# Kernel tuning notes

Measured on AMD Instinct MI355X. Metric: run time of the kernel, lower is better.

## Reference

```python
import jax, jax.numpy as jnp
import numpy as np

B, T, D = 4, 2048, 768
H = 12
DH = D // H
DFF = 3072
EPS = 1e-5


def _layernorm(x, g, b):
    mu = jnp.mean(x, axis=-1, keepdims=True)
    var = jnp.var(x, axis=-1, keepdims=True)
    return (x - mu) * jax.lax.rsqrt(var + EPS) * g + b


def setup_inputs() -> dict:
    key = jax.random.key(0)
    ks = jax.random.split(key, 12)
    s = lambda fan_in: 1.0 / np.sqrt(fan_in)
    return {
        "x": jax.random.normal(ks[0], (B, T, D), dtype=jnp.float32),
        "ln1_g": jnp.ones((D,), jnp.float32),
        "ln1_b": jnp.zeros((D,), jnp.float32),
        "w_qkv": jax.random.uniform(ks[1], (D, 3 * D), jnp.float32, -s(D), s(D)),
        "b_qkv": jax.random.uniform(ks[2], (3 * D,), jnp.float32, -s(D), s(D)),
        "w_proj": jax.random.uniform(ks[3], (D, D), jnp.float32, -s(D), s(D)),
        "b_proj": jax.random.uniform(ks[4], (D,), jnp.float32, -s(D), s(D)),
        "ln2_g": jnp.ones((D,), jnp.float32),
        "ln2_b": jnp.zeros((D,), jnp.float32),
        "w_ff1": jax.random.uniform(ks[5], (D, DFF), jnp.float32, -s(D), s(D)),
        "b_ff1": jax.random.uniform(ks[6], (DFF,), jnp.float32, -s(D), s(D)),
        "w_ff2": jax.random.uniform(ks[7], (DFF, D), jnp.float32, -s(DFF), s(DFF)),
        "b_ff2": jax.random.uniform(ks[8], (D,), jnp.float32, -s(DFF), s(DFF)),
    }


def reference(x, ln1_g, ln1_b, w_qkv, b_qkv, w_proj, b_proj,
              ln2_g, ln2_b, w_ff1, b_ff1, w_ff2, b_ff2):
    # --- attention sublayer ---
    h = _layernorm(x, ln1_g, ln1_b)
    qkv = h @ w_qkv + b_qkv                       # [B,T,3D]
    q, k, v = jnp.split(qkv, 3, axis=-1)
    q = q.reshape(B, T, H, DH).transpose(0, 2, 1, 3)  # [B,H,T,DH]
    k = k.reshape(B, T, H, DH).transpose(0, 2, 1, 3)
    v = v.reshape(B, T, H, DH).transpose(0, 2, 1, 3)
    att = jnp.einsum('bhqd,bhkd->bhqk', q, k) / jnp.sqrt(jnp.float32(DH))
    causal = jnp.tril(jnp.ones((T, T), dtype=bool))
    att = jnp.where(causal, att, -jnp.inf)
    att = jax.nn.softmax(att, axis=-1)
    out = jnp.einsum('bhqk,bhkd->bhqd', att, v)    # [B,H,T,DH]
    out = out.transpose(0, 2, 1, 3).reshape(B, T, D)
    x = x + out @ w_proj + b_proj
    # --- MLP sublayer ---
    h2 = _layernorm(x, ln2_g, ln2_b)
    h2 = jax.nn.gelu(h2 @ w_ff1 + b_ff1, approximate=False)
    x = x + h2 @ w_ff2 + b_ff2
    return x
```

## Files before the change

### kernel.cpp

```cpp
#include <hip/hip_runtime.h>
#include <cstdint>
#include <cstddef>

typedef unsigned short u16;
typedef unsigned int u32;
typedef __attribute__((ext_vector_type(8))) short s16x8;
typedef __attribute__((ext_vector_type(4))) float f32x4;

#define NB 4
#define NT 2048
#define ND 768
#define NH 12
#define NDH 64
#define NFF 3072
#define NM (NB*NT)

__device__ __forceinline__ u16 f2b(float f){
  union { float f; unsigned u; } c; c.f = f;
  unsigned r = c.u + 0x7fffu + ((c.u >> 16) & 1u);
  return (u16)(r >> 16);
}

__device__ __forceinline__ f32x4 mfma16(s16x8 a, s16x8 b, f32x4 c){
  return __builtin_amdgcn_mfma_f32_16x16x32_bf16(a, b, c, 0, 0, 0);
}

__device__ __forceinline__ void stage16(u16* lds, const u16* g){
  __builtin_amdgcn_global_load_lds(
      (const __attribute__((address_space(1))) unsigned int*)g,
      (__attribute__((address_space(3))) unsigned int*)lds,
      16, 0, 0);
}

__device__ __forceinline__ float gelu_f(float v){
  const float x = v * 0.70710678118654752f;
  const float ax = fabsf(x);
  const float t = 1.f / (1.f + 0.3275911f * ax);
  const float y = t * (0.254829592f + t * (-0.284496736f + t * (1.421413741f
                + t * (-1.453152027f + t * 1.061405429f))));
  float er = 1.f - y * __expf(-ax * ax);
  er = copysignf(er, x);
  return 0.5f * v * (1.f + er);
}

__global__ __launch_bounds__(256) void transpose_bf16(
    const float* __restrict__ in, u16* __restrict__ out, int K, int N)
{
  __shared__ float tile[32][33];
  const int n0 = blockIdx.x * 32, k0 = blockIdx.y * 32;
  const int tx = threadIdx.x, ty = threadIdx.y;
  #pragma unroll
  for (int i = 0; i < 32; i += 8)
    tile[ty + i][tx] = in[(size_t)(k0 + ty + i) * N + n0 + tx];
  __syncthreads();
  #pragma unroll
  for (int i = 0; i < 32; i += 8)
    out[(size_t)(n0 + ty + i) * K + k0 + tx] = f2b(tile[tx][ty + i]);
}

__global__ __launch_bounds__(256) void ln_kernel(
    const float* __restrict__ x, const float* __restrict__ g,
    const float* __restrict__ b, u16* __restrict__ out)
{
  const int row = blockIdx.x;
  const int t = threadIdx.x;
  const float* xr = x + (size_t)row * ND;
  float v0 = xr[t], v1 = xr[t + 256], v2 = xr[t + 512];
  float s = v0 + v1 + v2;
  float ss = v0*v0 + v1*v1 + v2*v2;
  #pragma unroll
  for (int o = 32; o; o >>= 1) { s += __shfl_xor(s, o, 64); ss += __shfl_xor(ss, o, 64); }
  __shared__ float red[8];
  const int w = t >> 6;
  if ((t & 63) == 0) { red[w] = s; red[4 + w] = ss; }
  __syncthreads();
  s  = red[0] + red[1] + red[2] + red[3];
  ss = red[4] + red[5] + red[6] + red[7];
  const float mu = s * (1.f / ND);
  const float var = ss * (1.f / ND) - mu * mu;
  const float rinv = rsqrtf(var + 1e-5f);
  u16* orow = out + (size_t)row * ND;
  orow[t]       = f2b((v0 - mu) * rinv * g[t]       + b[t]);
  orow[t + 256] = f2b((v1 - mu) * rinv * g[t + 256] + b[t + 256]);
  orow[t + 512] = f2b((v2 - mu) * rinv * g[t + 512] + b[t + 512]);
}

template<int EPI, int BM>
__global__ __launch_bounds__(256, (BM == 128) ? 3 : 4) void gemm_bt(
    const u16* __restrict__ A, const u16* __restrict__ Bt,
    const float* __restrict__ bias, const float* __restrict__ res,
    void* __restrict__ o0, void* __restrict__ o1, void* __restrict__ o2,
    const int M, const int N, const int K)
{
  constexpr int MI = BM / 64;
  __shared__ u16 As[3][BM * 32];
  __shared__ u16 Bs[3][128 * 32];
  const int tid = threadIdx.x;
  const int lane = tid & 63, wid = tid >> 6;
  const int wr = wid >> 1, wc = wid & 1;
  const int lg = lane >> 4, lm = lane & 15;
  const int bm = blockIdx.x * BM, bn = blockIdx.y * 128;

  f32x4 acc[2 * MI][4] = {};

  const int srow = tid >> 2;
  const int schunk = (tid & 3) ^ ((tid >> 3) & 3);
  const u16* ApT = A  + (size_t)(bm + srow) * K + schunk * 8;
  const u16* BpT = Bt + (size_t)(bn + srow) * K + schunk * 8;
  const size_t rs64 = (size_t)64 * K;
  const int woff = wid * 512;
  const int fswz = (lm >> 1) & 3;

  const int nt = K >> 5;

  #pragma unroll
  for (int p = 0; p < 2; ++p) {
    const int k0 = p << 5;
    stage16(&As[p][woff], ApT + k0);
    if (BM == 128) stage16(&As[p][woff + 2048], ApT + rs64 + k0);
    stage16(&Bs[p][woff],        BpT + k0);
    stage16(&Bs[p][woff + 2048], BpT + rs64 + k0);
  }

  for (int t = 0; t < nt; ++t) {
    if (t < nt - 1) {
      if (BM == 128) asm volatile("s_waitcnt vmcnt(4)" ::: "memory");
      else           asm volatile("s_waitcnt vmcnt(3)" ::: "memory");
    } else {
      asm volatile("s_waitcnt vmcnt(0)" ::: "memory");
    }
    __builtin_amdgcn_s_barrier();
    __builtin_amdgcn_sched_barrier(0);
    if (t + 2 < nt) {
      const int k0 = (t + 2) << 5;
      const int wb = (t + 2) % 3;
      stage16(&As[wb][woff], ApT + k0);
      if (BM == 128) stage16(&As[wb][woff + 2048], ApT + rs64 + k0);
      stage16(&Bs[wb][woff],        BpT + k0);
      stage16(&Bs[wb][woff + 2048], BpT + rs64 + k0);
    }
    __builtin_amdgcn_sched_barrier(0);
    const int rb = t % 3;
    s16x8 af[2 * MI], bf[4];
    #pragma unroll
    for (int i = 0; i < 2 * MI; i++)
      af[i] = *(const s16x8*)&As[rb][(wr * (BM / 2) + i * 16 + lm) * 32 + ((lg ^ fswz) * 8)];
    #pragma unroll
    for (int j = 0; j < 4; j++)
      bf[j] = *(const s16x8*)&Bs[rb][(wc * 64 + j * 16 + lm) * 32 + ((lg ^ fswz) * 8)];
    #pragma unroll
    for (int i = 0; i < 2 * MI; i++)
      #pragma unroll
      for (int j = 0; j < 4; j++)
        acc[i][j] = mfma16(af[i], bf[j], acc[i][j]);
  }

  #pragma unroll
  for (int i = 0; i < 2 * MI; i++)
    #pragma unroll
    for (int j = 0; j < 4; j++) {
      const int col = bn + wc * 64 + j * 16 + lm;
      const float bb = bias[col];
      #pragma unroll
      for (int r = 0; r < 4; r++) {
        const int row = bm + wr * (BM / 2) + i * 16 + lg * 4 + r;
        float v = acc[i][j][r] + bb;
        if (EPI == 0) {
          u16* dst; int rem;
          if (col < ND)            { dst = (u16*)o0; rem = col; v *= 0.125f; }
          else if (col < 2 * ND)   { dst = (u16*)o1; rem = col - ND; }
          else                     { dst = (u16*)o2; rem = col - 2 * ND; }
          const int hh = rem >> 6, dh = rem & 63;
          const int bb2 = row >> 11, tt = row & 2047;
          dst[(((size_t)bb2 * NH + hh) * NT + tt) * NDH + dh] = f2b(v);
        } else if (EPI == 1) {
          ((float*)o0)[(size_t)row * ND + col] = v + res[(size_t)row * ND + col];
        } else if (EPI == 2) {
          ((u16*)o0)[(size_t)row * NFF + col] = f2b(gelu_f(v));
        } else {
          ((float*)o0)[(size_t)row * ND + col] = v + res[(size_t)row * ND + col];
        }
      }
    }
}

__global__ __launch_bounds__(256,2) void attn_kernel(
    const u16* __restrict__ Q, const u16* __restrict__ Kg,
    const u16* __restrict__ V, u16* __restrict__ O)
{
  const int pairIdx = blockIdx.y;
  const int bh = blockIdx.x;
  const int b = bh / NH, h = bh % NH;
  const int tid = threadIdx.x;
  const int lane = tid & 63, w = tid >> 6;
  const int lg = lane >> 4, lm = lane & 15;
  const int sr = tid >> 3;
  const int sc = (tid & 7) * 8;

  __shared__ u16 Ks[64 * 64];
  __shared__ u16 Vt[64 * 64];
  __shared__ u16 Ps[4][16 * 64];

  const u16* Qb = Q  + (size_t)bh * NT * NDH;
  const u16* Kb = Kg + (size_t)bh * NT * NDH;
  const u16* Vb = V  + (size_t)bh * NT * NDH;

  for (int half = 0; half < 2; ++half) {
    const int si = half ? (31 - pairIdx) : pairIdx;
    const int q0 = si * 64;
    const int ktmax = si;

    const s16x8 qf0 = *(const s16x8*)&Qb[(size_t)(q0 + w * 16 + lm) * NDH + lg * 8];
    const s16x8 qf1 = *(const s16x8*)&Qb[(size_t)(q0 + w * 16 + lm) * NDH + 32 + lg * 8];

    f32x4 oacc[4] = {};
    float m = -INFINITY, l = 0.f;

    s16x8 kva = *(const s16x8*)&Kb[(size_t)sr * NDH + sc];
    s16x8 kvb = *(const s16x8*)&Kb[(size_t)(sr + 32) * NDH + sc];
    s16x8 vva = *(const s16x8*)&Vb[(size_t)sr * NDH + sc];
    s16x8 vvb = *(const s16x8*)&Vb[(size_t)(sr + 32) * NDH + sc];

    for (int kt = 0; kt <= ktmax; ++kt) {
      __syncthreads();
      *(s16x8*)&Ks[sr * 64 + (sc ^ ((sr & 7) << 3))] = kva;
      *(s16x8*)&Ks[(sr + 32) * 64 + (sc ^ ((sr & 7) << 3))] = kvb;
      #pragma unroll
      for (int e = 0; e < 8; ++e)
        Vt[(sc + e) * 64 + (sr ^ ((tid & 7) << 3))] = (u16)vva[e];
      #pragma unroll
      for (int e = 0; e < 8; ++e)
        Vt[(sc + e) * 64 + ((sr + 32) ^ ((tid & 7) << 3))] = (u16)vvb[e];
      __syncthreads();

      if (kt < ktmax) {
        const u16* Kn = Kb + (size_t)(kt + 1) * 64 * NDH;
        const u16* Vn = Vb + (size_t)(kt + 1) * 64 * NDH;
        kva = *(const s16x8*)&Kn[(size_t)sr * NDH + sc];
        kvb = *(const s16x8*)&Kn[(size_t)(sr + 32) * NDH + sc];
        vva = *(const s16x8*)&Vn[(size_t)sr * NDH + sc];
        vvb = *(const s16x8*)&Vn[(size_t)(sr + 32) * NDH + sc];
      }

      f32x4 sv[4];
      #pragma unroll
      for (int n = 0; n < 4; ++n) {
        const int krow = (n * 16 + lm) * 64;
        const int swz = (lm & 7) << 3;
        s16x8 kf0 = *(const s16x8*)&Ks[krow + ((lg * 8) ^ swz)];
        s16x8 kf1 = *(const s16x8*)&Ks[krow + ((32 + lg * 8) ^ swz)];
        f32x4 s4 = {};
        s4 = mfma16(kf0, qf0, s4);
        s4 = mfma16(kf1, qf1, s4);
        sv[n] = s4;
      }

      if (kt == ktmax) {
        #pragma unroll
        for (int n = 0; n < 4; ++n)
          #pragma unroll
          for (int r = 0; r < 4; ++r)
            if (n * 16 + lg * 4 + r > w * 16 + lm) sv[n][r] = -INFINITY;
      }

      float mx = -INFINITY;
      #pragma unroll
      for (int n = 0; n < 4; ++n)
        #pragma unroll
        for (int r = 0; r < 4; ++r) mx = fmaxf(mx, sv[n][r]);
      mx = fmaxf(mx, __shfl_xor(mx, 16));
      mx = fmaxf(mx, __shfl_xor(mx, 32));
      const float mnew = fmaxf(m, mx);
      const float alpha = __expf(m - mnew);
      m = mnew;

      float rs = 0.f;
      u32 pk[4][2];
      #pragma unroll
      for (int n = 0; n < 4; ++n) {
        const float p0 = __expf(sv[n][0] - mnew);
        const float p1 = __expf(sv[n][1] - mnew);
        const float p2 = __expf(sv[n][2] - mnew);
        const float p3 = __expf(sv[n][3] - mnew);
        rs += (p0 + p1) + (p2 + p3);
        pk[n][0] = (u32)f2b(p0) | ((u32)f2b(p1) << 16);
        pk[n][1] = (u32)f2b(p2) | ((u32)f2b(p3) << 16);
      }
      rs += __shfl_xor(rs, 16);
      rs += __shfl_xor(rs, 32);
      l = l * alpha + rs;

      #pragma unroll
      for (int n = 0; n < 4; ++n) {
        const int idx0 = lm * 64 + ((n * 16 + lg * 4) ^ ((lm & 7) << 3));
        *(u32*)&Ps[w][idx0] = pk[n][0];
        *(u32*)&Ps[w][idx0 + 2] = pk[n][1];
      }

      float av[4];
      #pragma unroll
      for (int r = 0; r < 4; ++r) av[r] = __shfl(alpha, lg * 4 + r);
      #pragma unroll
      for (int d = 0; d < 4; ++d)
        #pragma unroll
        for (int r = 0; r < 4; ++r) oacc[d][r] *= av[r];

      #pragma unroll
      for (int kh = 0; kh < 2; ++kh) {
        const s16x8 pf = *(const s16x8*)&Ps[w][lm * 64 + ((kh * 32 + lg * 8) ^ ((lm & 7) << 3))];
        #pragma unroll
        for (int dt = 0; dt < 4; ++dt) {
          const int g = (2 * dt + (lm >> 3)) & 7;
          const s16x8 vf = *(const s16x8*)&Vt[(dt * 16 + lm) * 64 + (((kh * 4 + lg) ^ g) << 3)];
          oacc[dt] = mfma16(pf, vf, oacc[dt]);
        }
      }
    }

    float lv[4];
    #pragma unroll
    for (int r = 0; r < 4; ++r) lv[r] = 1.f / __shfl(l, lg * 4 + r);
    #pragma unroll
    for (int dt = 0; dt < 4; ++dt)
      #pragma unroll
      for (int r = 0; r < 4; ++r) {
        const int qg = q0 + w * 16 + lg * 4 + r;
        O[((size_t)b * NT + qg) * ND + h * NDH + dt * 16 + lm] = f2b(oacc[dt][r] * lv[r]);
      }
  }
}

extern "C" void kernel_launch(void* const* d_in, const int* in_sizes, int n_in,
                              void* d_out, int out_size, void* d_ws, size_t ws_size,
                              hipStream_t stream)
{
  const float* x      = (const float*)d_in[0];
  const float* ln1_g  = (const float*)d_in[1];
  const float* ln1_b  = (const float*)d_in[2];
  const float* w_qkv  = (const float*)d_in[3];
  const float* b_qkv  = (const float*)d_in[4];
  const float* w_proj = (const float*)d_in[5];
  const float* b_proj = (const float*)d_in[6];
  const float* ln2_g  = (const float*)d_in[7];
  const float* ln2_b  = (const float*)d_in[8];
  const float* w_ff1  = (const float*)d_in[9];
  const float* b_ff1  = (const float*)d_in[10];
  const float* w_ff2  = (const float*)d_in[11];
  const float* b_ff2  = (const float*)d_in[12];

  char* ws = (char*)d_ws;
  u16*   wt_qkv = (u16*)(ws + 0);
  u16*   wt_proj= (u16*)(ws + 3538944);
  u16*   wt_ff1 = (u16*)(ws + 4718592);
  u16*   wt_ff2 = (u16*)(ws + 9437184);
  u16*   hbuf   = (u16*)(ws + 14155776);
  u16*   qbuf   = (u16*)(ws + 26738688);
  u16*   kbuf   = (u16*)(ws + 39321600);
  u16*   vbuf   = (u16*)(ws + 51904512);
  u16*   aobuf  = (u16*)(ws + 64487424);
  float* x1     = (float*)(ws + 77070336);
  u16*   h2buf  = (u16*)(ws + 102236160);
  u16*   ff1buf = hbuf;

  transpose_bf16<<<dim3(2304/32,  768/32), dim3(32,8), 0, stream>>>(w_qkv,  wt_qkv,  768, 2304);
  transpose_bf16<<<dim3( 768/32,  768/32), dim3(32,8), 0, stream>>>(w_proj, wt_proj, 768,  768);
  transpose_bf16<<<dim3(3072/32,  768/32), dim3(32,8), 0, stream>>>(w_ff1,  wt_ff1,  768, 3072);
  transpose_bf16<<<dim3( 768/32, 3072/32), dim3(32,8), 0, stream>>>(w_ff2,  wt_ff2, 3072,  768);

  ln_kernel<<<NM, 256, 0, stream>>>(x, ln1_g, ln1_b, hbuf);
  gemm_bt<0,128><<<dim3(NM/128, 2304/128), 256, 0, stream>>>(hbuf, wt_qkv, b_qkv, nullptr,
                                                             qbuf, kbuf, vbuf, NM, 2304, ND);
  attn_kernel<<<dim3(NB*NH, 16), 256, 0, stream>>>(qbuf, kbuf, vbuf, aobuf);
  gemm_bt<1,64><<<dim3(NM/64, ND/128), 256, 0, stream>>>(aobuf, wt_proj, b_proj, x,
                                                         x1, nullptr, nullptr, NM, ND, ND);
  ln_kernel<<<NM, 256, 0, stream>>>(x1, ln2_g, ln2_b, h2buf);
  gemm_bt<2,128><<<dim3(NM/128, NFF/128), 256, 0, stream>>>(h2buf, wt_ff1, b_ff1, nullptr,
                                                            ff1buf, nullptr, nullptr, NM, NFF, ND);
  gemm_bt<3,64><<<dim3(NM/64, ND/128), 256, 0, stream>>>(ff1buf, wt_ff2, b_ff2, x1,
                                                         d_out, nullptr, nullptr, NM, ND, NFF);
}
```

Before: 293.3 us.

## Add 256x256-tile 8-wave GEMM with grouped block order for QKV and FF1

Adds a new GEMM kernel with 512 threads and a 256x256 output tile that covers K in steps of 64, double-buffered in LDS. Block indices are remapped so neighbouring blocks share operand tiles. The MFMA work is split into four phases interleaved with LDS reads under s_setprio, and the kernel is used for the QKV and FF1 projections. This targets more reuse per loaded byte and better overlap of LDS loads with matrix ops, at the cost of higher register and LDS use, lower occupancy, and fewer blocks (288 and 384) across the CUs.

```diff
diff --git a/kernel.cpp b/kernel.cpp
--- a/kernel.cpp
+++ b/kernel.cpp
@@ -85,85 +85,136 @@
   orow[t + 512] = f2b((v2 - mu) * rinv * g[t + 512] + b[t + 512]);
 }
 
-template<int EPI, int BM>
-__global__ __launch_bounds__(256, (BM == 128) ? 3 : 4) void gemm_bt(
+template<int EPI>
+__global__ __launch_bounds__(512, 2) void gemm256(
     const u16* __restrict__ A, const u16* __restrict__ Bt,
-    const float* __restrict__ bias, const float* __restrict__ res,
+    const float* __restrict__ bias,
     void* __restrict__ o0, void* __restrict__ o1, void* __restrict__ o2,
-    const int M, const int N, const int K)
+    const int N, const int K)
 {
-  constexpr int MI = BM / 64;
-  __shared__ u16 As[3][BM * 32];
-  __shared__ u16 Bs[3][128 * 32];
+  __shared__ u16 Al[2][16384];
+  __shared__ u16 Bl[2][16384];
   const int tid = threadIdx.x;
   const int lane = tid & 63, wid = tid >> 6;
-  const int wr = wid >> 1, wc = wid & 1;
+  const int wm = wid >> 2, wn = wid & 3;
   const int lg = lane >> 4, lm = lane & 15;
-  const int bm = blockIdx.x * BM, bn = blockIdx.y * 128;
-
-  f32x4 acc[2 * MI][4] = {};
-
-  const int srow = tid >> 2;
-  const int schunk = (tid & 3) ^ ((tid >> 3) & 3);
-  const u16* ApT = A  + (size_t)(bm + srow) * K + schunk * 8;
-  const u16* BpT = Bt + (size_t)(bn + srow) * K + schunk * 8;
-  const size_t rs64 = (size_t)64 * K;
-  const int woff = wid * 512;
-  const int fswz = (lm >> 1) & 3;
-
-  const int nt = K >> 5;
+
+  const int nwg = gridDim.x * gridDim.y;
+  int bid = blockIdx.y * gridDim.x + blockIdx.x;
+  bid = (bid & 7) * (nwg >> 3) + (bid >> 3);
+  const int bm = (bid % gridDim.x) * 256;
+  const int bn = (bid / gridDim.x) * 256;
+
+  f32x4 acc[8][4] = {};
+
+  const int srow = (wid << 4) + (lane >> 2);
+  const int schunk = (lane & 3) ^ ((lane >> 3) & 3);
+  const u16* Ap = A  + (size_t)(bm + srow) * K + schunk * 8;
+  const u16* Bp = Bt + (size_t)(bn + srow) * K + schunk * 8;
+  const int wlds = wid << 9;
+
+  const int nkt = K >> 6;
+
+  auto STAGE = [&](int kt2) {
+    const int buf = kt2 & 1;
+    const size_t kof = (size_t)(kt2 << 6);
+    #pragma unroll
+    for (int h = 0; h < 2; ++h)
+      #pragma unroll
+      for (int L2 = 0; L2 < 2; ++L2) {
+        const size_t gofs = (size_t)(L2 << 7) * K + kof + (h << 5);
+        const int lofs = h * 8192 + L2 * 4096 + wlds;
+        stage16(&Al[buf][lofs], Ap + gofs);
+        stage16(&Bl[buf][lofs], Bp + gofs);
+      }
+  };
+
+  auto LDA = [&](int buf, int rf, int ks) -> s16x8 {
+    const int r = (wm << 7) + (rf << 4) + lm;
+    const int s = lg ^ ((lm >> 1) & 3);
+    return *(const s16x8*)&Al[buf][(ks << 13) + (r << 5) + (s << 3)];
+  };
+  auto LDB = [&](int buf, int cf, int ks) -> s16x8 {
+    const int r = (wn << 6) + (cf << 4) + lm;
+    const int s = lg ^ ((lm >> 1) & 3);
+    return *(const s16x8*)&Bl[buf][(ks << 13) + (r << 5) + (s << 3)];
+  };
+
+  STAGE(0);
+
+  for (int kt = 0; kt < nkt; ++kt) {
+    const int buf = kt & 1;
+    asm volatile("s_waitcnt vmcnt(0)" ::: "memory");
+    __builtin_amdgcn_s_barrier();
+
+    s16x8 a0[4][2], b0[2][2];
+    #pragma unroll
+    for (int i = 0; i < 4; ++i) { a0[i][0] = LDA(buf, i, 0); a0[i][1] = LDA(buf, i, 1); }
+    #pragma unroll
+    for (int j = 0; j < 2; ++j) { b0[j][0] = LDB(buf, j, 0); b0[j][1] = LDB(buf, j, 1); }
+    if (kt + 1 < nkt) STAGE(kt + 1);
+    __builtin_amdgcn_s_barrier();
+    __builtin_amdgcn_s_setprio(1);
+    #pragma unroll
+    for (int i = 0; i < 4; ++i)
+      #pragma unroll
+      for (int j = 0; j < 2; ++j) {
+        acc[i][j] = mfma16(a0[i][0], b0[j][0], acc[i][j]);
+        acc[i][j] = mfma16(a0[i][1], b0[j][1], acc[i][j]);
+      }
+    __builtin_amdgcn_s_setprio(0);
+    __builtin_amdgcn_s_barrier();
+
+    s16x8 b1[2][2];
+    #pragma unroll
+    for (int j = 0; j < 2; ++j) { b1[j][0] = LDB(buf, 2 + j, 0); b1[j][1] = LDB(buf, 2 + j, 1); }
+    __builtin_amdgcn_s_barrier();
+    __builtin_amdgcn_s_setprio(1);
+    #pragma unroll
+    for (int i = 0; i < 4; ++i)
+      #pragma unroll
+      for (int j = 0; j < 2; ++j) {
+        acc[i][2 + j] = mfma16(a0[i][0], b1[j][0], acc[i][2 + j]);
+        acc[i][2 + j] = mfma16(a0[i][1], b1[j][1], acc[i][2 + j]);
+      }
+    __builtin_amdgcn_s_setprio(0);
+    __builtin_amdgcn_s_barrier();
+
+    s16x8 a1[4][2];
+    #pragma unroll
+    for (int i = 0; i < 4; ++i) { a1[i][0] = LDA(buf, 4 + i, 0); a1[i][1] = LDA(buf, 4 + i, 1); }
+    __builtin_amdgcn_s_barrier();
+    __builtin_amdgcn_s_setprio(1);
+    #pragma unroll
+    for (int i = 0; i < 4; ++i)
+      #pragma unroll
+      for (int j = 0; j < 2; ++j) {
+        acc[4 + i][2 + j] = mfma16(a1[i][0], b1[j][0], acc[4 + i][2 + j]);
+        acc[4 + i][2 + j] = mfma16(a1[i][1], b1[j][1], acc[4 + i][2 + j]);
+      }
+    __builtin_amdgcn_s_setprio(0);
+    __builtin_amdgcn_s_barrier();
+
+    __builtin_amdgcn_s_setprio(1);
+    #pragma unroll
+    for (int i = 0; i < 4; ++i)
+      #pragma unroll
+      for (int j = 0; j < 2; ++j) {
+        acc[4 + i][j] = mfma16(a1[i][0], b0[j][0], acc[4 + i][j]);
+        acc[4 + i][j] = mfma16(a1[i][1], b0[j][1], acc[4 + i][j]);
+      }
+    __builtin_amdgcn_s_setprio(0);
+  }
 
   #pragma unroll
-  for (int p = 0; p < 2; ++p) {
-    const int k0 = p << 5;
-    stage16(&As[p][woff], ApT + k0);
-    if (BM == 128) stage16(&As[p][woff + 2048], ApT + rs64 + k0);
-    stage16(&Bs[p][woff],        BpT + k0);
-    stage16(&Bs[p][woff + 2048], BpT + rs64 + k0);
-  }
-
-  for (int t = 0; t < nt; ++t) {
-    if (t < nt - 1) {
-      if (BM == 128) asm volatile("s_waitcnt vmcnt(4)" ::: "memory");
-      else           asm volatile("s_waitcnt vmcnt(3)" ::: "memory");
-    } else {
-      asm volatile("s_waitcnt vmcnt(0)" ::: "memory");
-    }
-    __builtin_amdgcn_s_barrier();
-    __builtin_amdgcn_sched_barrier(0);
-    if (t + 2 < nt) {
-      const int k0 = (t + 2) << 5;
-      const int wb = (t + 2) % 3;
-      stage16(&As[wb][woff], ApT + k0);
-      if (BM == 128) stage16(&As[wb][woff + 2048], ApT + rs64 + k0);
-      stage16(&Bs[wb][woff],        BpT + k0);
-      stage16(&Bs[wb][woff + 2048], BpT + rs64 + k0);
-    }
-    __builtin_amdgcn_sched_barrier(0);
-    const int rb = t % 3;
-    s16x8 af[2 * MI], bf[4];
-    #pragma unroll
-    for (int i = 0; i < 2 * MI; i++)
-      af[i] = *(const s16x8*)&As[rb][(wr * (BM / 2) + i * 16 + lm) * 32 + ((lg ^ fswz) * 8)];
-    #pragma unroll
-    for (int j = 0; j < 4; j++)
-      bf[j] = *(const s16x8*)&Bs[rb][(wc * 64 + j * 16 + lm) * 32 + ((lg ^ fswz) * 8)];
-    #pragma unroll
-    for (int i = 0; i < 2 * MI; i++)
-      #pragma unroll
-      for (int j = 0; j < 4; j++)
-        acc[i][j] = mfma16(af[i], bf[j], acc[i][j]);
-  }
-
-  #pragma unroll
-  for (int i = 0; i < 2 * MI; i++)
-    #pragma unroll
-    for (int j = 0; j < 4; j++) {
-      const int col = bn + wc * 64 + j * 16 + lm;
+  for (int i = 0; i < 8; ++i)
+    #pragma unroll
+    for (int j = 0; j < 4; ++j) {
+      const int col = bn + (wn << 6) + (j << 4) + lm;
       const float bb = bias[col];
       #pragma unroll
-      for (int r = 0; r < 4; r++) {
-        const int row = bm + wr * (BM / 2) + i * 16 + lg * 4 + r;
+      for (int r = 0; r < 4; ++r) {
+        const int row = bm + (wm << 7) + (i << 4) + (lg << 2) + r;
         float v = acc[i][j][r] + bb;
         if (EPI == 0) {
           u16* dst; int rem;
@@ -173,13 +224,86 @@
           const int hh = rem >> 6, dh = rem & 63;
           const int bb2 = row >> 11, tt = row & 2047;
           dst[(((size_t)bb2 * NH + hh) * NT + tt) * NDH + dh] = f2b(v);
-        } else if (EPI == 1) {
-          ((float*)o0)[(size_t)row * ND + col] = v + res[(size_t)row * ND + col];
-        } else if (EPI == 2) {
+        } else {
           ((u16*)o0)[(size_t)row * NFF + col] = f2b(gelu_f(v));
-        } else {
-          ((float*)o0)[(size_t)row * ND + col] = v + res[(size_t)row * ND + col];
         }
+      }
+    }
+}
+
+template<int EPI>
+__global__ __launch_bounds__(256, 4) void gemm_bt(
+    const u16* __restrict__ A, const u16* __restrict__ Bt,
+    const float* __restrict__ bias, const float* __restrict__ res,
+    void* __restrict__ o0, const int M, const int N, const int K)
+{
+  __shared__ u16 As[3][64 * 32];
+  __shared__ u16 Bs[3][128 * 32];
+  const int tid = threadIdx.x;
+  const int lane = tid & 63, wid = tid >> 6;
+  const int wr = wid >> 1, wc = wid & 1;
+  const int lg = lane >> 4, lm = lane & 15;
+  const int bm = blockIdx.x * 64, bn = blockIdx.y * 128;
+
+  f32x4 acc[2][4] = {};
+
+  const int srow = tid >> 2;
+  const int schunk = (tid & 3) ^ ((tid >> 3) & 3);
+  const u16* ApT = A  + (size_t)(bm + srow) * K + schunk * 8;
+  const u16* BpT = Bt + (size_t)(bn + srow) * K + schunk * 8;
+  const size_t rs64 = (size_t)64 * K;
+  const int woff = wid * 512;
+  const int fswz = (lm >> 1) & 3;
+
+  const int nt = K >> 5;
+
+  #pragma unroll
+  for (int p = 0; p < 2; ++p) {
+    const int k0 = p << 5;
+    stage16(&As[p][woff], ApT + k0);
+    stage16(&Bs[p][woff],        BpT + k0);
+    stage16(&Bs[p][woff + 2048], BpT + rs64 + k0);
+  }
+
+  for (int t = 0; t < nt; ++t) {
+    if (t < nt - 1) asm volatile("s_waitcnt vmcnt(3)" ::: "memory");
+    else            asm volatile("s_waitcnt vmcnt(0)" ::: "memory");
+    __builtin_amdgcn_s_barrier();
+    __builtin_amdgcn_sched_barrier(0);
+    if (t + 2 < nt) {
+      const int k0 = (t + 2) << 5;
+      const int wb = (t + 2) % 3;
+      stage16(&As[wb][woff], ApT + k0);
+      stage16(&Bs[wb][woff],        BpT + k0);
+      stage16(&Bs[wb][woff + 2048], BpT + rs64 + k0);
+    }
+    __builtin_amdgcn_sched_barrier(0);
+    const int rb = t % 3;
+    s16x8 af[2], bf[4];
+    #pragma unroll
+    for (int i = 0; i < 2; i++)
+      af[i] = *(const s16x8*)&As[rb][(wr * 32 + i * 16 + lm) * 32 + ((lg ^ fswz) * 8)];
+    #pragma unroll
+    for (int j = 0; j < 4; j++)
+      bf[j] = *(const s16x8*)&Bs[rb][(wc * 64 + j * 16 + lm) * 32 + ((lg ^ fswz) * 8)];
+    #pragma unroll
+    for (int i = 0; i < 2; i++)
+      #pragma unroll
+      for (int j = 0; j < 4; j++)
+        acc[i][j] = mfma16(af[i], bf[j], acc[i][j]);
+  }
+
+  #pragma unroll
+  for (int i = 0; i < 2; i++)
+    #pragma unroll
+    for (int j = 0; j < 4; j++) {
+      const int col = bn + wc * 64 + j * 16 + lm;
+      const float bb = bias[col];
+      #pragma unroll
+      for (int r = 0; r < 4; r++) {
+        const int row = bm + wr * 32 + i * 16 + lg * 4 + r;
+        const float v = acc[i][j][r] + bb;
+        ((float*)o0)[(size_t)row * ND + col] = v + res[(size_t)row * ND + col];
       }
     }
 }
@@ -368,14 +492,14 @@
   transpose_bf16<<<dim3( 768/32, 3072/32), dim3(32,8), 0, stream>>>(w_ff2,  wt_ff2, 3072,  768);
 
   ln_kernel<<<NM, 256, 0, stream>>>(x, ln1_g, ln1_b, hbuf);
-  gemm_bt<0,128><<<dim3(NM/128, 2304/128), 256, 0, stream>>>(hbuf, wt_qkv, b_qkv, nullptr,
-                                                             qbuf, kbuf, vbuf, NM, 2304, ND);
+  gemm256<0><<<dim3(NM/256, 2304/256), 512, 0, stream>>>(hbuf, wt_qkv, b_qkv,
+                                                         qbuf, kbuf, vbuf, 2304, ND);
   attn_kernel<<<dim3(NB*NH, 16), 256, 0, stream>>>(qbuf, kbuf, vbuf, aobuf);
-  gemm_bt<1,64><<<dim3(NM/64, ND/128), 256, 0, stream>>>(aobuf, wt_proj, b_proj, x,
-                                                         x1, nullptr, nullptr, NM, ND, ND);
+  gemm_bt<1><<<dim3(NM/64, ND/128), 256, 0, stream>>>(aobuf, wt_proj, b_proj, x,
+                                                      x1, NM, ND, ND);
   ln_kernel<<<NM, 256, 0, stream>>>(x1, ln2_g, ln2_b, h2buf);
-  gemm_bt<2,128><<<dim3(NM/128, NFF/128), 256, 0, stream>>>(h2buf, wt_ff1, b_ff1, nullptr,
-                                                            ff1buf, nullptr, nullptr, NM, NFF, ND);
-  gemm_bt<3,64><<<dim3(NM/64, ND/128), 256, 0, stream>>>(ff1buf, wt_ff2, b_ff2, x1,
-                                                         d_out, nullptr, nullptr, NM, ND, NFF);
-}
+  gemm256<2><<<dim3(NM/256, NFF/256), 512, 0, stream>>>(h2buf, wt_ff1, b_ff1,
+                                                        ff1buf, nullptr, nullptr, NFF, ND);
+  gemm_bt<3><<<dim3(NM/64, ND/128), 256, 0, stream>>>(ff1buf, wt_ff2, b_ff2, x1,
+                                                      d_out, NM, ND, NFF);
+}
```

Result: slower. 339.8 us (+15.8%).
